# Kernel tuning notes

Hardware: AMD Instinct MI355X
Metric: run time of the kernel (lower is better)

Reference implementation:

```python
import jax, jax.numpy as jnp
import numpy as np

DIM = 256
HEADS = 8
HD = DIM // HEADS          # 32
WS = 8                     # window size
TOPK = 4
SCALE = HD ** -0.5


def setup_inputs() -> dict:
    key = jax.random.key(0)
    k1, k2, k3 = jax.random.split(key, 3)
    B, H, W = 8, 64, 64
    x = jax.random.normal(k1, (B, DIM, H, W), dtype=jnp.float32)
    # 1x1 conv weights (BN folded -> weight + bias), fan-in scaled to keep logits sane
    w_qkv = jax.random.normal(k2, (3 * DIM, DIM), dtype=jnp.float32) / np.sqrt(DIM)
    b_qkv = jnp.zeros((3 * DIM,), dtype=jnp.float32)
    w_proj = jax.random.normal(k3, (DIM, DIM), dtype=jnp.float32) / np.sqrt(DIM)
    b_proj = jnp.zeros((DIM,), dtype=jnp.float32)
    return {"x": x, "w_qkv": w_qkv, "b_qkv": b_qkv, "w_proj": w_proj, "b_proj": b_proj}


def _window_partition(t, ws):
    # t: [BH, D, H, W] -> [BH, R, ws*ws, D]
    bh, d, h, w = t.shape
    gh, gw = h // ws, w // ws
    t = t.reshape(bh, d, gh, ws, gw, ws)
    t = t.transpose(0, 2, 4, 3, 5, 1)          # [BH, gh, gw, ws, ws, D]
    return t.reshape(bh, gh * gw, ws * ws, d)


def reference(x, w_qkv, b_qkv, w_proj, b_proj):
    B, C, H, W = x.shape
    gh, gw = H // WS, W // WS
    R, T = gh * gw, WS * WS
    BH = B * HEADS

    # qkv 1x1 conv
    qkv = jnp.einsum('bchw,oc->bohw', x, w_qkv) + b_qkv[None, :, None, None]
    q, k, v = jnp.split(qkv, 3, axis=1)                       # each [B, C, H, W]

    def to_bh(t):
        return t.reshape(BH, HD, H, W)

    q_w = _window_partition(to_bh(q), WS)                     # [BH, R, T, HD]
    k_w = _window_partition(to_bh(k), WS)
    v_w = _window_partition(to_bh(v), WS)

    # region-level routing: mean-pooled region tokens
    q_r = q_w.mean(axis=2)                                    # [BH, R, HD]
    k_r = k_w.mean(axis=2)
    attn_r = jnp.einsum('brd,bkd->brk', q_r, k_r) * SCALE     # [BH, R, R]
    topk = min(TOPK, R)
    _, topk_idx = jax.lax.top_k(attn_r, topk)                 # [BH, R, K]

    # gather top-k key/value windows per query region
    bidx = jnp.arange(BH)[:, None, None]
    k_sel = k_w[bidx, topk_idx]                               # [BH, R, K, T, HD]
    v_sel = v_w[bidx, topk_idx]
    k_sel = k_sel.reshape(BH, R, topk * T, HD)
    v_sel = v_sel.reshape(BH, R, topk * T, HD)

    # token-level attention inside routed regions
    attn = jnp.einsum('brtd,brsd->brts', q_w, k_sel) * SCALE  # [BH, R, T, K*T]
    attn = jax.nn.softmax(attn, axis=-1)
    out_w = jnp.einsum('brts,brsd->brtd', attn, v_sel)        # [BH, R, T, HD]

    # window reverse -> [BH, HD, H, W]
    out = out_w.reshape(BH, gh, gw, WS, WS, HD)
    out = out.transpose(0, 5, 1, 3, 2, 4).reshape(BH, HD, H, W)
    out = out.reshape(B, C, H, W)

    out = jnp.einsum('bchw,oc->bohw', out, w_proj) + b_proj[None, :, None, None]
    return out
```

## Files before the change

kernel.cpp:

```cpp
#include <hip/hip_runtime.h>
#include <hip/hip_bf16.h>

#define ATT_SCALE 0.17677669529663687f
#define EXP_C1 0.2550349235534668f
#define EXP_C2 23.083120654223400f

typedef short v8s __attribute__((ext_vector_type(8)));
typedef float v4f __attribute__((ext_vector_type(4)));
typedef float v16f __attribute__((ext_vector_type(16)));
typedef const __attribute__((address_space(1))) unsigned int gu32;
typedef __attribute__((address_space(3))) unsigned int lu32;

__device__ __forceinline__ void g2l16(const void* g, void* l) {
  __builtin_amdgcn_global_load_lds((gu32*)g, (lu32*)l, 16, 0, 0);
}

__device__ __forceinline__ float bflo(unsigned u){ union{unsigned i;float f;}x; x.i=u<<16; return x.f; }
__device__ __forceinline__ float bfhi(unsigned u){ union{unsigned i;float f;}x; x.i=u&0xffff0000u; return x.f; }
__device__ __forceinline__ unsigned short bf16r(float v){
  __hip_bfloat16 h = __float2bfloat16(v);
  return *reinterpret_cast<unsigned short*>(&h);
}
__device__ __forceinline__ unsigned pack_bf2(float a, float b){
  return (unsigned)bf16r(a) | ((unsigned)bf16r(b) << 16);
}
__device__ __forceinline__ unsigned cvtpk(float lo, float hi){
  unsigned r;
  asm("v_cvt_pk_bf16_f32 %0, %1, %2" : "=v"(r) : "v"(lo), "v"(hi));
  return r;
}
__device__ __forceinline__ void pl32swap(unsigned &a, unsigned &b){
  asm volatile("v_permlane32_swap_b32 %0, %1" : "+v"(a), "+v"(b));
}

__global__ __launch_bounds__(256) void k_prep(const float* __restrict__ x,
                                              const float* __restrict__ w_qkv,
                                              const float* __restrict__ w_proj,
                                              unsigned short* __restrict__ Xb,
                                              unsigned short* __restrict__ Wq,
                                              unsigned short* __restrict__ Wp,
                                              float* __restrict__ part) {
  __shared__ __align__(16) char hbuf[8192];
  __shared__ float pbuf[512];
  const int blk = blockIdx.x;
  const int t = threadIdx.x;
  if (blk >= 2048) {
    const int m = blk - 2048;
    const float* src = (m < 768) ? (w_qkv + m*256) : (w_proj + (size_t)(m - 768)*256);
    unsigned short* dst = (m < 768) ? (Wq + m*256) : (Wp + (size_t)(m - 768)*256);
    int col = (t & ~63) | ((t & 63) ^ ((m & 7) << 3));
    dst[col] = bf16r(src[t]);
    return;
  }
  const int b = blk >> 8, cc = (blk >> 6) & 3, pc = blk & 63;
  const int c0 = cc << 6, p0 = pc << 6;
  const int wv = t >> 6, lane = t & 63;

  float hi[16];
  const float* xp = x + ((size_t)(b*256 + c0 + wv*16))*4096 + p0 + lane;
  #pragma unroll
  for (int i = 0; i < 16; ++i) hi[i] = xp[(size_t)i*4096];

  #pragma unroll
  for (int i = 0; i < 16; ++i) {
    float s = hi[i];
    s += __shfl_xor(s, 1);
    s += __shfl_xor(s, 2);
    s += __shfl_xor(s, 4);
    if ((lane & 7) == 0) pbuf[(wv*16 + i)*8 + (lane >> 3)] = s;
  }

  #pragma unroll
  for (int gi = 0; gi < 2; ++gi) {
    uint4 uh;
    uh.x = pack_bf2(hi[gi*8+0], hi[gi*8+1]); uh.y = pack_bf2(hi[gi*8+2], hi[gi*8+3]);
    uh.z = pack_bf2(hi[gi*8+4], hi[gi*8+5]); uh.w = pack_bf2(hi[gi*8+6], hi[gi*8+7]);
    int off = lane*128 + ((wv*32 + gi*16) ^ ((lane & 7) << 4));
    *(uint4*)(hbuf + off) = uh;
  }
  __syncthreads();
  const size_t rowbase = ((size_t)(b*4096 + p0)) * 512 + (size_t)c0*2;
  #pragma unroll
  for (int s = 0; s < 2; ++s) {
    int gidx = s*256 + t;
    int row = gidx >> 3, gb = (gidx & 7) << 4;
    uint4 vh = *(const uint4*)(hbuf + row*128 + gb);
    *(uint4*)((char*)Xb + rowbase + (size_t)row*512 + gb) = vh;
  }
  const size_t pbase = ((size_t)(b*64 + pc)*256 + c0)*8;
  part[pbase + t]       = pbuf[t];
  part[pbase + 256 + t] = pbuf[t + 256];
}

__global__ __launch_bounds__(256) void k_xmr(const float* __restrict__ part,
                                             float* __restrict__ xmean) {
  const int blk = blockIdx.x;
  const int item = blk & 7;
  const int b = blk >> 6, rh = (blk >> 3) & 7;
  const int t = threadIdx.x;
  const int flat = item*256 + t;
  float acc = 0.f;
  const float* pp = part + (size_t)(b*64 + rh*8)*2048 + flat;
  #pragma unroll
  for (int j = 0; j < 8; ++j) acc += pp[(size_t)j*2048];
  const int c = flat >> 3, wc = flat & 7;
  xmean[(size_t)((b*256 + c) << 6) + (rh << 3) + wc] = acc * 0.015625f;
}

__global__ __launch_bounds__(256) void k_route(const float* __restrict__ xmean,
                                               const float* __restrict__ w_qkv,
                                               const float* __restrict__ b_qkv,
                                               int* __restrict__ topk) {
  __shared__ float xm[128][64];
  __shared__ float qr[64][33];
  __shared__ float kr[64][33];
  const int bh = blockIdx.x, b = bh >> 3, head = bh & 7;
  const int tid = threadIdx.x;
  const int d = tid & 31, r0 = tid >> 5;
  float qacc[8], kacc[8];
  const float bq = b_qkv[head*32 + d], bk = b_qkv[256 + head*32 + d];
  #pragma unroll
  for (int i = 0; i < 8; ++i) { qacc[i] = bq; kacc[i] = bk; }

  for (int c0 = 0; c0 < 256; c0 += 128) {
    __syncthreads();
    #pragma unroll
    for (int i = 0; i < 32; ++i) {
      int idx = i*256 + tid;
      int row = idx >> 6, col = idx & 63;
      xm[row][col] = xmean[(size_t)(b*256 + c0 + row)*64 + col];
    }
    __syncthreads();
    const float* wqp = w_qkv + (head*32 + d)*256 + c0;
    const float* wkp = w_qkv + (256 + head*32 + d)*256 + c0;
    for (int c = 0; c < 128; ++c) {
      float wq = wqp[c], wk = wkp[c];
      #pragma unroll
      for (int i = 0; i < 8; ++i) {
        float xv = xm[c][r0 + 8*i];
        qacc[i] += wq * xv;
        kacc[i] += wk * xv;
      }
    }
  }
  #pragma unroll
  for (int i = 0; i < 8; ++i) { qr[r0+8*i][d] = qacc[i]; kr[r0+8*i][d] = kacc[i]; }
  __syncthreads();

  float* ar = &xm[0][0];
  for (int item = tid; item < 4096; item += 256) {
    int i = item >> 6, j = item & 63;
    float s = 0.f;
    #pragma unroll
    for (int dd = 0; dd < 32; ++dd) s += qr[i][dd]*kr[j][dd];
    ar[i*64 + j] = s;
  }
  __syncthreads();
  if (tid < 64) {
    for (int kk = 0; kk < 4; ++kk) {
      float best = -3e38f; int bj = 0;
      for (int j = 0; j < 64; ++j) {
        float v = ar[tid*64 + j];
        if (v > best) { best = v; bj = j; }
      }
      ar[tid*64 + bj] = -3e38f;
      topk[(bh*64 + tid)*4 + kk] = bj;
    }
  }
}

template<int EPI>
__global__ __launch_bounds__(256) void k_gemm(
    const unsigned short* __restrict__ Wstk,
    const unsigned short* __restrict__ Bmat,
    const float* __restrict__ bias,
    unsigned short* __restrict__ qbuf, unsigned short* __restrict__ kbuf,
    unsigned short* __restrict__ vbuf, float* __restrict__ outp) {
  __shared__ __align__(16) char lds[49152];
  const int tid = threadIdx.x;
  const int wv = tid >> 6, lane = tid & 63;
  const int mt = blockIdx.x, nt = blockIdx.y;

  v4f acc[2][4];
  #pragma unroll
  for (int i = 0; i < 2; ++i)
    #pragma unroll
    for (int j = 0; j < 4; ++j) acc[i][j] = (v4f){0.f,0.f,0.f,0.f};

  const char* wlanebase = (const char*)Wstk + ((size_t)(mt*128) + (lane>>3))*512 + (lane&7)*16;
  const char* xlanebase = (const char*)Bmat + ((size_t)(nt*64 + (lane>>3))*512 + (lane&7)*16);

  {
    char* wb = lds; char* xb = lds + 32768;
    #pragma unroll
    for (int o = 0; o < 4; ++o) { int op = wv*4 + o; g2l16(wlanebase + (size_t)(op*8)*512, wb + op*1024); }
    #pragma unroll
    for (int o = 0; o < 2; ++o) { int op = wv*2 + o; g2l16(xlanebase + (size_t)(op*8)*512, xb + op*1024); }
  }
  asm volatile("s_waitcnt vmcnt(0)" ::: "memory");
  __syncthreads();

  int cur = 0;
  #pragma unroll
  for (int kt = 0; kt < 4; ++kt) {
    if (kt < 3) {
      const int k0b = (kt + 1)*128;
      char* wb = lds + (cur^1)*16384;
      char* xb = lds + 32768 + (cur^1)*8192;
      #pragma unroll
      for (int o = 0; o < 4; ++o) { int op = wv*4 + o; g2l16(wlanebase + (size_t)(op*8)*512 + k0b, wb + op*1024); }
      #pragma unroll
      for (int o = 0; o < 2; ++o) { int op = wv*2 + o; g2l16(xlanebase + (size_t)(op*8)*512 + k0b, xb + op*1024); }
    }
    {
      const char* wb = lds + cur*16384;
      const char* xb = lds + 32768 + cur*8192;
      #pragma unroll
      for (int kk = 0; kk < 2; ++kk) {
        const int kb = kk*64 + ((lane>>4)<<4);
        v8s a[2], b[4];
        #pragma unroll
        for (int i = 0; i < 2; ++i) {
          int mr = wv*32 + i*16 + (lane & 15);
          a[i] = *(const v8s*)(wb + mr*128 + (kb ^ ((mr & 7) << 4)));
        }
        #pragma unroll
        for (int j = 0; j < 4; ++j) {
          int nr = j*16 + (lane & 15);
          b[j] = *(const v8s*)(xb + nr*128 + (kb ^ ((nr & 7) << 4)));
        }
        #pragma unroll
        for (int i = 0; i < 2; ++i)
          #pragma unroll
          for (int j = 0; j < 4; ++j)
            acc[i][j] = __builtin_amdgcn_mfma_f32_16x16x32_bf16(a[i], b[j], acc[i][j], 0, 0, 0);
      }
    }
    if (kt < 3) {
      asm volatile("s_waitcnt vmcnt(0)" ::: "memory");
      __syncthreads();
      cur ^= 1;
    }
  }

  if (EPI == 0) {
    if (mt < 4) {
      unsigned short* outbuf = (mt < 2) ? qbuf : kbuf;
      #pragma unroll
      for (int i = 0; i < 2; ++i) {
        int o = mt*128 + wv*32 + i*16 + ((lane >> 4) << 2);
        int head = (o >> 5) & 7, d0 = o & 31;
        float b0 = bias[o], b1 = bias[o+1], b2 = bias[o+2], b3 = bias[o+3];
        #pragma unroll
        for (int j = 0; j < 4; ++j) {
          int p = nt*64 + j*16 + (lane & 15);
          int bb = p >> 12, ploc = p & 4095;
          int h = ploc >> 6, w = ploc & 63;
          int rr = ((h >> 3) << 3) | (w >> 3), tt = ((h & 7) << 3) | (w & 7);
          int bh = bb*8 + head;
          uint2 u;
          u.x = pack_bf2(acc[i][j][0] + b0, acc[i][j][1] + b1);
          u.y = pack_bf2(acc[i][j][2] + b2, acc[i][j][3] + b3);
          *(uint2*)(outbuf + (size_t)(((bh << 6) | rr)*64 + tt)*32 + d0) = u;
        }
      }
    } else {
      #pragma unroll
      for (int i = 0; i < 2; ++i) {
        int o = mt*128 + wv*32 + i*16 + ((lane >> 4) << 2);
        int vch = o - 512;
        int head = vch >> 5, d0 = vch & 31;
        float bv[4] = {bias[o], bias[o+1], bias[o+2], bias[o+3]};
        #pragma unroll
        for (int j = 0; j < 4; ++j) {
          int p = nt*64 + j*16 + (lane & 15);
          int bb = p >> 12, ploc = p & 4095;
          int h = ploc >> 6, w = ploc & 63;
          int rr = ((h >> 3) << 3) | (w >> 3), tt = ((h & 7) << 3) | (w & 7);
          int bh = bb*8 + head;
          size_t base = ((size_t)((bh << 6) | rr)*32 + d0)*64 + tt;
          #pragma unroll
          for (int c = 0; c < 4; ++c)
            vbuf[base + (size_t)c*64] = bf16r(acc[i][j][c] + bv[c]);
        }
      }
    }
  } else {
    #pragma unroll
    for (int i = 0; i < 2; ++i) {
      int o = mt*128 + wv*32 + i*16 + ((lane >> 4) << 2);
      float b0 = bias[o], b1 = bias[o+1], b2 = bias[o+2], b3 = bias[o+3];
      #pragma unroll
      for (int j = 0; j < 4; ++j) {
        int p = nt*64 + j*16 + (lane & 15);
        int bb = p >> 12, ploc = p & 4095;
        float* dst = outp + ((size_t)(bb*256 + o))*4096 + ploc;
        dst[0]     = acc[i][j][0] + b0;
        dst[4096]  = acc[i][j][1] + b1;
        dst[8192]  = acc[i][j][2] + b2;
        dst[12288] = acc[i][j][3] + b3;
      }
    }
  }
}

__global__ __launch_bounds__(256) void k_attn(const unsigned short* __restrict__ qw,
                                              const unsigned short* __restrict__ kw,
                                              const unsigned short* __restrict__ vwt,
                                              const int* __restrict__ topk,
                                              unsigned short* __restrict__ owt) {
  const int lane = threadIdx.x & 63;
  const int W = blockIdx.x*4 + (threadIdx.x >> 6);
  const int bh = W >> 6, rr = W & 63;
  const int lo5 = lane & 31, hi = lane >> 5;
  const int b = bh >> 3, head = bh & 7;

  const unsigned short* qb = qw + (size_t)(bh*64 + rr)*2048;
  v8s qf[2][2];
  #pragma unroll
  for (int qt = 0; qt < 2; ++qt)
    #pragma unroll
    for (int ck = 0; ck < 2; ++ck)
      qf[qt][ck] = *(const v8s*)(qb + (qt*32 + lo5)*32 + ck*16 + hi*8);

  int idx4[4];
  #pragma unroll
  for (int w = 0; w < 4; ++w) idx4[w] = topk[(bh*64 + rr)*4 + w];

  v16f O[2];
  #pragma unroll
  for (int qt = 0; qt < 2; ++qt)
    #pragma unroll
    for (int r = 0; r < 16; ++r) O[qt][r] = 0.f;
  float lsum[2] = {0.f, 0.f};

  #pragma unroll
  for (int w = 0; w < 4; ++w) {
    const unsigned short* kb = kw  + (size_t)(bh*64 + idx4[w])*2048;
    const unsigned short* vb = vwt + (size_t)(bh*64 + idx4[w])*2048;
    v8s kf[2][2], vf[4];
    #pragma unroll
    for (int kt = 0; kt < 2; ++kt)
      #pragma unroll
      for (int ck = 0; ck < 2; ++ck)
        kf[kt][ck] = *(const v8s*)(kb + (kt*32 + lo5)*32 + ck*16 + hi*8);
    #pragma unroll
    for (int mk = 0; mk < 4; ++mk)
      vf[mk] = *(const v8s*)(vb + lo5*64 + mk*16 + hi*8);

    v16f S[2][2];
    #pragma unroll
    for (int kt = 0; kt < 2; ++kt)
      #pragma unroll
      for (int qt = 0; qt < 2; ++qt) {
        v16f z;
        #pragma unroll
        for (int r = 0; r < 16; ++r) z[r] = 0.f;
        z = __builtin_amdgcn_mfma_f32_32x32x16_bf16(kf[kt][0], qf[qt][0], z, 0, 0, 0);
        S[kt][qt] = __builtin_amdgcn_mfma_f32_32x32x16_bf16(kf[kt][1], qf[qt][1], z, 0, 0, 0);
      }

    #pragma unroll
    for (int kt = 0; kt < 2; ++kt) {
      #pragma unroll
      for (int qt = 0; qt < 2; ++qt) {
        float p[16];
        #pragma unroll
        for (int r = 0; r < 16; ++r)
          p[r] = __builtin_amdgcn_exp2f(__builtin_fmaf(S[kt][qt][r], EXP_C1, -EXP_C2));
        float s01 = (p[0]+p[1]) + (p[2]+p[3]);
        float s23 = (p[4]+p[5]) + (p[6]+p[7]);
        float s45 = (p[8]+p[9]) + (p[10]+p[11]);
        float s67 = (p[12]+p[13]) + (p[14]+p[15]);
        lsum[qt] += (s01 + s23) + (s45 + s67);

        unsigned wh[8], wl[8];
        #pragma unroll
        for (int i = 0; i < 8; ++i) {
          wh[i] = cvtpk(p[2*i], p[2*i+1]);
          float l0 = p[2*i]   - bflo(wh[i]);
          float l1 = p[2*i+1] - bfhi(wh[i]);
          wl[i] = cvtpk(l0, l1);
        }
        pl32swap(wh[0], wh[2]); pl32swap(wh[1], wh[3]);
        pl32swap(wh[4], wh[6]); pl32swap(wh[5], wh[7]);
        pl32swap(wl[0], wl[2]); pl32swap(wl[1], wl[3]);
        pl32swap(wl[4], wl[6]); pl32swap(wl[5], wl[7]);
        union { unsigned u[4]; v8s v; } fA, fB;
        fA.u[0] = wh[0]; fA.u[1] = wh[1]; fA.u[2] = wh[2]; fA.u[3] = wh[3];
        fB.u[0] = wl[0]; fB.u[1] = wl[1]; fB.u[2] = wl[2]; fB.u[3] = wl[3];
        O[qt] = __builtin_amdgcn_mfma_f32_32x32x16_bf16(fA.v, vf[2*kt], O[qt], 0, 0, 0);
        O[qt] = __builtin_amdgcn_mfma_f32_32x32x16_bf16(fB.v, vf[2*kt], O[qt], 0, 0, 0);
        fA.u[0] = wh[4]; fA.u[1] = wh[5]; fA.u[2] = wh[6]; fA.u[3] = wh[7];
        fB.u[0] = wl[4]; fB.u[1] = wl[5]; fB.u[2] = wl[6]; fB.u[3] = wl[7];
        O[qt] = __builtin_amdgcn_mfma_f32_32x32x16_bf16(fA.v, vf[2*kt+1], O[qt], 0, 0, 0);
        O[qt] = __builtin_amdgcn_mfma_f32_32x32x16_bf16(fB.v, vf[2*kt+1], O[qt], 0, 0, 0);
      }
    }
  }

  float linv[2];
  #pragma unroll
  for (int qt = 0; qt < 2; ++qt) {
    float t = lsum[qt] + __shfl_xor(lsum[qt], 32);
    linv[qt] = 1.0f / t;
  }

  #pragma unroll
  for (int qt = 0; qt < 2; ++qt) {
    #pragma unroll
    for (int r = 0; r < 16; ++r) {
      int q = (r & 3) + 8*(r >> 2) + 4*hi;
      float li = __shfl(linv[qt], q);
      float val = O[qt][r] * li;
      int tok = qt*32 + q;
      int h = ((rr >> 3) << 3) | (tok >> 3);
      int wcol = ((rr & 7) << 3) | (tok & 7);
      int pg = (b << 12) | (h << 6) | wcol;
      int col = ((head >> 1) << 6) | ((((head & 1) << 5) + lo5) ^ ((tok & 7) << 3));
      owt[(size_t)pg*256 + col] = bf16r(val);
    }
  }
}

extern "C" void kernel_launch(void* const* d_in, const int* in_sizes, int n_in,
                              void* d_out, int out_size, void* d_ws, size_t ws_size,
                              hipStream_t stream) {
  (void)in_sizes; (void)n_in; (void)out_size; (void)ws_size;
  const float* x      = (const float*)d_in[0];
  const float* w_qkv  = (const float*)d_in[1];
  const float* b_qkv  = (const float*)d_in[2];
  const float* w_proj = (const float*)d_in[3];
  const float* b_proj = (const float*)d_in[4];
  float* out = (float*)d_out;

  char* ws = (char*)d_ws;
  unsigned short* Xb  = (unsigned short*)ws;
  unsigned short* Wq  = (unsigned short*)(ws + 16777216);
  unsigned short* Wp  = (unsigned short*)(ws + 17170432);
  unsigned short* qw  = (unsigned short*)(ws + 17301504);
  unsigned short* kw  = (unsigned short*)(ws + 34078720);
  unsigned short* vwt = (unsigned short*)(ws + 50855936);
  float* part         = (float*)(ws + 67633152);
  float* xmean        = (float*)(ws + 71827456);
  int* topk           = (int*)(ws + 72351744);
  unsigned short* owt = Xb;

  k_prep <<<dim3(3072), 256, 0, stream>>>(x, w_qkv, w_proj, Xb, Wq, Wp, part);
  k_xmr  <<<dim3(512),  256, 0, stream>>>(part, xmean);
  k_route<<<dim3(64),   256, 0, stream>>>(xmean, w_qkv, b_qkv, topk);
  k_gemm<0><<<dim3(6, 512), 256, 0, stream>>>(Wq, Xb, b_qkv, qw, kw, vwt, nullptr);
  k_attn <<<dim3(1024), 256, 0, stream>>>(qw, kw, vwt, topk, owt);
  k_gemm<1><<<dim3(2, 512), 256, 0, stream>>>(Wp, owt, b_proj, nullptr, nullptr, nullptr, out);
}
```

Baseline: 122.8 us.

## Load GEMM weight fragments straight to registers and swap grid axes

The GEMM kernels no longer stage the weight tile through LDS. Each lane reads its A fragments directly from global memory, which lets the weight swizzle in k_prep be dropped and shrinks LDS from 48KB to 16KB, raising possible occupancy. The grid axes are also swapped so that consecutive blocks share the same weight tile and walk across N, which should improve cache reuse of the weights. The cost is a global-load latency on the A fragments inside the k-loop with no double buffering for them.

```diff
diff --git a/kernel.cpp b/kernel.cpp
--- a/kernel.cpp
+++ b/kernel.cpp
@@ -48,8 +48,7 @@
     const int m = blk - 2048;
     const float* src = (m < 768) ? (w_qkv + m*256) : (w_proj + (size_t)(m - 768)*256);
     unsigned short* dst = (m < 768) ? (Wq + m*256) : (Wp + (size_t)(m - 768)*256);
-    int col = (t & ~63) | ((t & 63) ^ ((m & 7) << 3));
-    dst[col] = bf16r(src[t]);
+    dst[t] = bf16r(src[t]);
     return;
   }
   const int b = blk >> 8, cc = (blk >> 6) & 3, pc = blk & 63;
@@ -176,10 +175,10 @@
     const float* __restrict__ bias,
     unsigned short* __restrict__ qbuf, unsigned short* __restrict__ kbuf,
     unsigned short* __restrict__ vbuf, float* __restrict__ outp) {
-  __shared__ __align__(16) char lds[49152];
+  __shared__ __align__(16) char lds[16384];
   const int tid = threadIdx.x;
   const int wv = tid >> 6, lane = tid & 63;
-  const int mt = blockIdx.x, nt = blockIdx.y;
+  const int nt = blockIdx.x, mt = blockIdx.y;
 
   v4f acc[2][4];
   #pragma unroll
@@ -187,16 +186,12 @@
     #pragma unroll
     for (int j = 0; j < 4; ++j) acc[i][j] = (v4f){0.f,0.f,0.f,0.f};
 
-  const char* wlanebase = (const char*)Wstk + ((size_t)(mt*128) + (lane>>3))*512 + (lane&7)*16;
+  const char* wrowbase = (const char*)Wstk
+      + ((size_t)(mt*128 + wv*32 + (lane & 15)))*512 + ((lane >> 4) << 4);
   const char* xlanebase = (const char*)Bmat + ((size_t)(nt*64 + (lane>>3))*512 + (lane&7)*16);
 
-  {
-    char* wb = lds; char* xb = lds + 32768;
-    #pragma unroll
-    for (int o = 0; o < 4; ++o) { int op = wv*4 + o; g2l16(wlanebase + (size_t)(op*8)*512, wb + op*1024); }
-    #pragma unroll
-    for (int o = 0; o < 2; ++o) { int op = wv*2 + o; g2l16(xlanebase + (size_t)(op*8)*512, xb + op*1024); }
-  }
+  #pragma unroll
+  for (int o = 0; o < 2; ++o) { int op = wv*2 + o; g2l16(xlanebase + (size_t)(op*8)*512, lds + op*1024); }
   asm volatile("s_waitcnt vmcnt(0)" ::: "memory");
   __syncthreads();
 
@@ -204,37 +199,31 @@
   #pragma unroll
   for (int kt = 0; kt < 4; ++kt) {
     if (kt < 3) {
-      const int k0b = (kt + 1)*128;
-      char* wb = lds + (cur^1)*16384;
-      char* xb = lds + 32768 + (cur^1)*8192;
-      #pragma unroll
-      for (int o = 0; o < 4; ++o) { int op = wv*4 + o; g2l16(wlanebase + (size_t)(op*8)*512 + k0b, wb + op*1024); }
-      #pragma unroll
-      for (int o = 0; o < 2; ++o) { int op = wv*2 + o; g2l16(xlanebase + (size_t)(op*8)*512 + k0b, xb + op*1024); }
-    }
-    {
-      const char* wb = lds + cur*16384;
-      const char* xb = lds + 32768 + cur*8192;
-      #pragma unroll
-      for (int kk = 0; kk < 2; ++kk) {
-        const int kb = kk*64 + ((lane>>4)<<4);
-        v8s a[2], b[4];
-        #pragma unroll
-        for (int i = 0; i < 2; ++i) {
-          int mr = wv*32 + i*16 + (lane & 15);
-          a[i] = *(const v8s*)(wb + mr*128 + (kb ^ ((mr & 7) << 4)));
-        }
-        #pragma unroll
-        for (int j = 0; j < 4; ++j) {
-          int nr = j*16 + (lane & 15);
-          b[j] = *(const v8s*)(xb + nr*128 + (kb ^ ((nr & 7) << 4)));
-        }
-        #pragma unroll
-        for (int i = 0; i < 2; ++i)
-          #pragma unroll
-          for (int j = 0; j < 4; ++j)
-            acc[i][j] = __builtin_amdgcn_mfma_f32_16x16x32_bf16(a[i], b[j], acc[i][j], 0, 0, 0);
-      }
+      char* xb = lds + (cur^1)*8192;
+      #pragma unroll
+      for (int o = 0; o < 2; ++o) { int op = wv*2 + o; g2l16(xlanebase + (size_t)(op*8)*512 + (kt+1)*128, xb + op*1024); }
+    }
+    v8s a[2][2];
+    #pragma unroll
+    for (int kk = 0; kk < 2; ++kk)
+      #pragma unroll
+      for (int i = 0; i < 2; ++i)
+        a[kk][i] = *(const v8s*)(wrowbase + (size_t)(i*16)*512 + kt*128 + kk*64);
+    const char* xb = lds + cur*8192;
+    #pragma unroll
+    for (int kk = 0; kk < 2; ++kk) {
+      const int kb = kk*64 + ((lane>>4)<<4);
+      v8s b[4];
+      #pragma unroll
+      for (int j = 0; j < 4; ++j) {
+        int nr = j*16 + (lane & 15);
+        b[j] = *(const v8s*)(xb + nr*128 + (kb ^ ((nr & 7) << 4)));
+      }
+      #pragma unroll
+      for (int i = 0; i < 2; ++i)
+        #pragma unroll
+        for (int j = 0; j < 4; ++j)
+          acc[i][j] = __builtin_amdgcn_mfma_f32_16x16x32_bf16(a[kk][i], b[j], acc[i][j], 0, 0, 0);
     }
     if (kt < 3) {
       asm volatile("s_waitcnt vmcnt(0)" ::: "memory");
@@ -449,7 +438,7 @@
   k_prep <<<dim3(3072), 256, 0, stream>>>(x, w_qkv, w_proj, Xb, Wq, Wp, part);
   k_xmr  <<<dim3(512),  256, 0, stream>>>(part, xmean);
   k_route<<<dim3(64),   256, 0, stream>>>(xmean, w_qkv, b_qkv, topk);
-  k_gemm<0><<<dim3(6, 512), 256, 0, stream>>>(Wq, Xb, b_qkv, qw, kw, vwt, nullptr);
+  k_gemm<0><<<dim3(512, 6), 256, 0, stream>>>(Wq, Xb, b_qkv, qw, kw, vwt, nullptr);
   k_attn <<<dim3(1024), 256, 0, stream>>>(qw, kw, vwt, topk, owt);
-  k_gemm<1><<<dim3(2, 512), 256, 0, stream>>>(Wp, owt, b_proj, nullptr, nullptr, nullptr, out);
-}
+  k_gemm<1><<<dim3(512, 2), 256, 0, stream>>>(Wp, owt, b_proj, nullptr, nullptr, nullptr, out);
+}
```

After: 129.3 us. 1.05x slower.
